# Performance work log

Hardware: AMD Instinct MI355X
Metric: run time of the kernel (lower is better)

The kernel has to match this reference:

```python
import jax, jax.numpy as jnp
import numpy as np

STATE_DIM = 28224  # 84*84*4 flattened Atari stack
N_EPISODE = 8192
FEATURE_DIM = 32
K_NEAREST = 10
C = 0.001
EPS_KERNEL = 0.001


def setup_inputs() -> dict:
    key = jax.random.key(0)
    ks = jax.random.split(key, 5)
    s = jax.random.normal(ks[0], (1, STATE_DIM), dtype=jnp.float32)
    episode = jax.random.normal(ks[1], (N_EPISODE, STATE_DIM), dtype=jnp.float32)
    dm2 = jnp.ones((1,), dtype=jnp.float32)  # running distance stat (torch inits 0.0; 1.0 avoids div-by-zero)
    # fan-in scaled weights so activations stay O(1)
    W1 = jax.random.normal(ks[2], (STATE_DIM, 128), dtype=jnp.float32) / np.sqrt(STATE_DIM)
    b1 = jnp.zeros((128,), dtype=jnp.float32)
    W2 = jax.random.normal(ks[3], (128, 64), dtype=jnp.float32) / np.sqrt(128.0)
    b2 = jnp.zeros((64,), dtype=jnp.float32)
    W3 = jax.random.normal(ks[4], (64, FEATURE_DIM), dtype=jnp.float32) / np.sqrt(64.0)
    b3 = jnp.zeros((FEATURE_DIM,), dtype=jnp.float32)
    return {"s": s, "episode": episode, "dm2": dm2,
            "W1": W1, "b1": b1, "W2": W2, "b2": b2, "W3": W3, "b3": b3}


def _embed(x, W1, b1, W2, b2, W3, b3):
    h = jax.nn.relu(x @ W1 + b1)
    h = jax.nn.relu(h @ W2 + b2)
    return h @ W3 + b3  # [*, FEATURE_DIM]


def reference(s, episode, dm2, W1, b1, W2, b2, W3, b3):
    z_s = _embed(s, W1, b1, W2, b2, W3, b3)          # [1, F]
    z_ep = _embed(episode, W1, b1, W2, b2, W3, b3)   # [N, F]
    dist = jnp.linalg.norm(z_s - z_ep, axis=1)       # [N]
    kernel = EPS_KERNEL / (dist / dm2[0] + EPS_KERNEL)
    top_k_kernel, _ = jax.lax.top_k(kernel, K_NEAREST)           # largest kernel values
    neg_top_dist, _ = jax.lax.top_k(-dist, K_NEAREST)            # smallest distances
    top_k_dist = -neg_top_dist
    new_dm2 = 0.99 * dm2[0] + 0.01 * jnp.mean(top_k_dist)        # running-stat update
    reward_episodic = 1.0 / (jnp.sqrt(jnp.mean(top_k_kernel)) + C)
    return reward_episodic, new_dm2
```

## Files before the change

kernel.cpp:

```cpp
#include <hip/hip_runtime.h>
#include <hip/hip_bf16.h>

typedef __attribute__((ext_vector_type(8))) __bf16 bf16x8;
typedef __attribute__((ext_vector_type(4))) float f32x4;
typedef __attribute__((ext_vector_type(4))) unsigned short u16x4;

#define STATE_DIM 28224
#define NEP 8192
#define MPAD 8320
#define KSPLIT 7
#define KSTEPS 63
#define BK 64
#define EPSK 0.001f
#define CC 0.001f

#define WT_BYTES   (441 * 8192 * 2)
#define PART_BYTES (KSPLIT * MPAD * 128 * 4)
#define Z_BYTES    (MPAD * 32 * 4)
#define DIST_BYTES (NEP * 4)
#define WS_NEEDED  (WT_BYTES + PART_BYTES + Z_BYTES + DIST_BYTES)

__device__ __forceinline__ unsigned short f2bf(float f) {
    unsigned int u = __float_as_uint(f);
    u += 0x7fffu + ((u >> 16) & 1u);
    return (unsigned short)(u >> 16);
}

__device__ __forceinline__ void glds16(const void* g, void* l) {
    __builtin_amdgcn_global_load_lds(
        (const __attribute__((address_space(1))) unsigned int*)g,
        (__attribute__((address_space(3))) unsigned int*)l, 16, 0, 0);
}

__global__ __launch_bounds__(256) void prep_wt(const float* __restrict__ W1,
                                               unsigned short* __restrict__ WtS) {
    __shared__ __align__(16) unsigned short img[8192];
    const int c = blockIdx.x;
    const int tid = threadIdx.x;
    const int k0 = c * 64;
#pragma unroll
    for (int i = 0; i < 32; ++i) {
        const int f = i * 256 + tid;
        const int k = f >> 7, n = f & 127;
        const float wv = W1[(size_t)(k0 + k) * 128 + n];
        const int ad = ((n * 128 + k * 2) ^ ((n & 7) << 4)) >> 1;
        img[ad] = f2bf(wv);
    }
    __syncthreads();
    unsigned short* dst = WtS + (size_t)c * 8192;
#pragma unroll
    for (int i = 0; i < 4; ++i) {
        const int f = i * 256 + tid;
        *reinterpret_cast<uint4*>(dst + f * 8) =
            *reinterpret_cast<const uint4*>(img + f * 8);
    }
}

__global__ __launch_bounds__(256, 3) void gemm1(const float* __restrict__ ep,
                                                const float* __restrict__ s,
                                                const unsigned short* __restrict__ WtS,
                                                float* __restrict__ part) {
    __shared__ __align__(16) unsigned char smA[128 * 64 * 2];
    __shared__ __align__(16) unsigned char smB[2][128 * 64 * 2];

    const int bid = blockIdx.x;
    const int ks = bid / 65;
    const int mt = bid % 65;
    const int tid = threadIdx.x;
    const int kBase = ks * (KSTEPS * BK);
    const int chunkBase = ks * KSTEPS;

    const int mBase = tid >> 4;
    const int kOff = (tid & 15) * 4;
    const int swzW = (mBase & 7) << 4;

    const bool last = (mt == 64);
    const int rowBase = mt * 128;

    float4 aR[8];

    auto loadA = [&](int kc) {
#pragma unroll
        for (int i = 0; i < 8; ++i) {
            const int m = mBase + i * 16;
            const int rg = rowBase + m;
            if (!last) {
                aR[i] = *reinterpret_cast<const float4*>(ep + (size_t)rg * STATE_DIM + kc + kOff);
            } else {
                if (rg < NEP)
                    aR[i] = *reinterpret_cast<const float4*>(ep + (size_t)rg * STATE_DIM + kc + kOff);
                else if (rg == NEP)
                    aR[i] = *reinterpret_cast<const float4*>(s + kc + kOff);
                else
                    aR[i] = make_float4(0.f, 0.f, 0.f, 0.f);
            }
        }
    };

    const int w = tid >> 6;
    const int lane = tid & 63;

    auto stageB = [&](int chunkIdx, int buf) {
        const char* cb = (const char*)(WtS + (size_t)chunkIdx * 8192);
#pragma unroll
        for (int r2 = 0; r2 < 4; ++r2) {
            const int off = ((r2 << 2) + w) << 10;
            glds16(cb + off + (lane << 4), &smB[buf][off]);
        }
    };

    auto writeLdsA = [&]() {
#pragma unroll
        for (int i = 0; i < 8; ++i) {
            const int m = mBase + i * 16;
            u16x4 av;
            av[0] = f2bf(aR[i].x); av[1] = f2bf(aR[i].y);
            av[2] = f2bf(aR[i].z); av[3] = f2bf(aR[i].w);
            const int ad = (m * 128 + kOff * 2) ^ swzW;
            *reinterpret_cast<u16x4*>(smA + ad) = av;
        }
    };

    const int wr = w >> 1, wc = w & 1;
    const int l15 = lane & 15, lq = lane >> 4;
    const int swzF = (l15 & 7) << 4;

    f32x4 acc[4][4] = {};

    auto compute = [&](int buf) {
#pragma unroll
        for (int kh = 0; kh < 2; ++kh) {
            bf16x8 af[4], bf[4];
#pragma unroll
            for (int mf = 0; mf < 4; ++mf) {
                const int row = wr * 64 + mf * 16 + l15;
                const int ad = (row * 128 + (kh * 32 + lq * 8) * 2) ^ swzF;
                af[mf] = *reinterpret_cast<const bf16x8*>(smA + ad);
            }
#pragma unroll
            for (int nf = 0; nf < 4; ++nf) {
                const int row = wc * 64 + nf * 16 + l15;
                const int ad = (row * 128 + (kh * 32 + lq * 8) * 2) ^ swzF;
                bf[nf] = *reinterpret_cast<const bf16x8*>(smB[buf] + ad);
            }
#pragma unroll
            for (int mf = 0; mf < 4; ++mf)
#pragma unroll
                for (int nf = 0; nf < 4; ++nf)
                    acc[mf][nf] = __builtin_amdgcn_mfma_f32_16x16x32_bf16(
                        af[mf], bf[nf], acc[mf][nf], 0, 0, 0);
        }
    };

    loadA(kBase);
    stageB(chunkBase, 0);
    int buf = 0;
    for (int t2 = 0; t2 < KSTEPS; ++t2) {
        __syncthreads();
        writeLdsA();
        __syncthreads();
        if (t2 + 1 < KSTEPS) {
            loadA(kBase + (t2 + 1) * BK);
            stageB(chunkBase + t2 + 1, buf ^ 1);
        }
        compute(buf);
        buf ^= 1;
    }

    float* po = part + ((size_t)ks * MPAD + rowBase) * 128;
#pragma unroll
    for (int mf = 0; mf < 4; ++mf)
#pragma unroll
        for (int nf = 0; nf < 4; ++nf)
#pragma unroll
            for (int v = 0; v < 4; ++v) {
                const int row = wr * 64 + mf * 16 + lq * 4 + v;
                const int col = wc * 64 + nf * 16 + l15;
                po[(size_t)row * 128 + col] = acc[mf][nf][v];
            }
}

__global__ __launch_bounds__(256) void mlp23(const float* __restrict__ part,
                                             const float* __restrict__ b1,
                                             const float* __restrict__ W2,
                                             const float* __restrict__ b2,
                                             const float* __restrict__ W3,
                                             const float* __restrict__ b3,
                                             float* __restrict__ z) {
    __shared__ float W2t[64 * 129];
    __shared__ float W3t[32 * 65];
    __shared__ float b1L[128], b2L[64], b3L[32];
    __shared__ float h1buf[4][128];
    __shared__ float h2buf[4][64];

    const int tid = threadIdx.x;
#pragma unroll
    for (int i = 0; i < 32; ++i) {
        int f = tid + i * 256;
        W2t[(f & 63) * 129 + (f >> 6)] = W2[f];
    }
#pragma unroll
    for (int i = 0; i < 8; ++i) {
        int f = tid + i * 256;
        W3t[(f & 31) * 65 + (f >> 5)] = W3[f];
    }
    if (tid < 128) b1L[tid] = b1[tid];
    if (tid < 64) b2L[tid] = b2[tid];
    if (tid < 32) b3L[tid] = b3[tid];
    __syncthreads();

    const int w = tid >> 6, l = tid & 63;
    const int base = blockIdx.x * 16 + w * 4;
    for (int rr = 0; rr < 4; ++rr) {
        const int r = base + rr;
        if (r > NEP) continue;
        float h1a = b1L[l], h1b = b1L[l + 64];
#pragma unroll
        for (int p = 0; p < KSPLIT; ++p) {
            const float* pp = part + ((size_t)p * MPAD + r) * 128;
            h1a += pp[l];
            h1b += pp[l + 64];
        }
        h1a = fmaxf(h1a, 0.f);
        h1b = fmaxf(h1b, 0.f);
        h1buf[w][l] = h1a;
        h1buf[w][l + 64] = h1b;
        float s0 = 0.f, s1 = 0.f, s2 = 0.f, s3 = 0.f;
        const float* wr2 = &W2t[l * 129];
        const float* hb = h1buf[w];
#pragma unroll 8
        for (int k = 0; k < 32; ++k) {
            s0 += hb[k]      * wr2[k];
            s1 += hb[k + 32] * wr2[k + 32];
            s2 += hb[k + 64] * wr2[k + 64];
            s3 += hb[k + 96] * wr2[k + 96];
        }
        float a2 = fmaxf(b2L[l] + ((s0 + s1) + (s2 + s3)), 0.f);
        h2buf[w][l] = a2;
        const int c = l & 31;
        const float* wr3 = &W3t[c * 65];
        const float* h2 = h2buf[w];
        float t0 = 0.f, t1 = 0.f;
#pragma unroll 8
        for (int k = 0; k < 32; ++k) {
            t0 += h2[k]      * wr3[k];
            t1 += h2[k + 32] * wr3[k + 32];
        }
        if (l < 32) z[(size_t)r * 32 + c] = b3L[c] + t0 + t1;
    }
}

__global__ __launch_bounds__(256) void dist_k(const float* __restrict__ z,
                                              float* __restrict__ dist) {
    __shared__ float zs[32];
    const int t = threadIdx.x;
    if (t < 32) zs[t] = z[(size_t)NEP * 32 + t];
    __syncthreads();
    const int r = blockIdx.x * 256 + t;
    const float* zr = z + (size_t)r * 32;
    float d2 = 0.f;
#pragma unroll
    for (int c2 = 0; c2 < 32; ++c2) {
        const float d = zr[c2] - zs[c2];
        d2 += d * d;
    }
    dist[r] = sqrtf(d2);
}

__global__ __launch_bounds__(256) void top10_k(const float* __restrict__ dist,
                                               const float* __restrict__ dm2,
                                               float* __restrict__ out) {
    const int t = threadIdx.x;
    float v[32];
#pragma unroll
    for (int i = 0; i < 32; ++i) v[i] = dist[i * 256 + t];

    __shared__ float wv[4];
    __shared__ int wi[4];

    const float dm = dm2[0];
    float sd = 0.f, sk = 0.f;

    for (int round = 0; round < 10; ++round) {
        float bv = 3.0e38f;
        int bi = 0x7fffffff;
#pragma unroll
        for (int i = 0; i < 32; ++i) {
            const float x = v[i];
            const int idx = i * 256 + t;
            if (x < bv) { bv = x; bi = idx; }
        }
#pragma unroll
        for (int sft = 1; sft < 64; sft <<= 1) {
            const float ov = __shfl_xor(bv, sft);
            const int oi = __shfl_xor(bi, sft);
            if (ov < bv || (ov == bv && oi < bi)) { bv = ov; bi = oi; }
        }
        const int wid = t >> 6;
        if ((t & 63) == 0) { wv[wid] = bv; wi[wid] = bi; }
        __syncthreads();
        bv = wv[0]; bi = wi[0];
#pragma unroll
        for (int k = 1; k < 4; ++k) {
            const float ov = wv[k]; const int oi = wi[k];
            if (ov < bv || (ov == bv && oi < bi)) { bv = ov; bi = oi; }
        }
        __syncthreads();
#pragma unroll
        for (int i = 0; i < 32; ++i)
            if (bi == i * 256 + t) v[i] = 3.0e38f;
        sd += bv;
        sk += EPSK / (bv / dm + EPSK);
    }

    if (t == 0) {
        const float meand = sd * 0.1f;
        const float meank = sk * 0.1f;
        out[0] = 1.0f / (sqrtf(meank) + CC);
        out[1] = 0.99f * dm + 0.01f * meand;
    }
}

extern "C" void kernel_launch(void* const* d_in, const int* in_sizes, int n_in,
                              void* d_out, int out_size, void* d_ws, size_t ws_size,
                              hipStream_t stream) {
    const float* s   = (const float*)d_in[0];
    const float* ep  = (const float*)d_in[1];
    const float* dm2 = (const float*)d_in[2];
    const float* W1  = (const float*)d_in[3];
    const float* b1  = (const float*)d_in[4];
    const float* W2  = (const float*)d_in[5];
    const float* b2  = (const float*)d_in[6];
    const float* W3  = (const float*)d_in[7];
    const float* b3  = (const float*)d_in[8];
    float* out = (float*)d_out;

    if (ws_size < (size_t)WS_NEEDED) return;

    unsigned short* WtS = (unsigned short*)d_ws;
    float* part = (float*)((char*)d_ws + WT_BYTES);
    float* zbuf = (float*)((char*)d_ws + WT_BYTES + PART_BYTES);
    float* dist = (float*)((char*)d_ws + WT_BYTES + PART_BYTES + Z_BYTES);

    hipLaunchKernelGGL(prep_wt, dim3(441), dim3(256), 0, stream, W1, WtS);
    hipLaunchKernelGGL(gemm1, dim3(65 * KSPLIT), dim3(256), 0, stream, ep, s, WtS, part);
    hipLaunchKernelGGL(mlp23, dim3(MPAD / 16), dim3(256), 0, stream, part, b1, W2, b2, W3, b3, zbuf);
    hipLaunchKernelGGL(dist_k, dim3(32), dim3(256), 0, stream, zbuf, dist);
    hipLaunchKernelGGL(top10_k, dim3(1), dim3(256), 0, stream, dist, dm2, out);
}
```

Baseline: 241.4 us.

## Store GEMM1 split-K partials as bf16 and remap workgroups across XCDs

```diff
diff --git a/kernel.cpp b/kernel.cpp
--- a/kernel.cpp
+++ b/kernel.cpp
@@ -11,11 +11,12 @@
 #define KSPLIT 7
 #define KSTEPS 63
 #define BK 64
+#define NWG (65 * KSPLIT)
 #define EPSK 0.001f
 #define CC 0.001f
 
 #define WT_BYTES   (441 * 8192 * 2)
-#define PART_BYTES (KSPLIT * MPAD * 128 * 4)
+#define PART_BYTES (KSPLIT * MPAD * 128 * 2)
 #define Z_BYTES    (MPAD * 32 * 4)
 #define DIST_BYTES (NEP * 4)
 #define WS_NEEDED  (WT_BYTES + PART_BYTES + Z_BYTES + DIST_BYTES)
@@ -56,14 +57,18 @@
     }
 }
 
-__global__ __launch_bounds__(256, 3) void gemm1(const float* __restrict__ ep,
+__global__ __launch_bounds__(256, 2) void gemm1(const float* __restrict__ ep,
                                                 const float* __restrict__ s,
                                                 const unsigned short* __restrict__ WtS,
-                                                float* __restrict__ part) {
+                                                unsigned short* __restrict__ part) {
     __shared__ __align__(16) unsigned char smA[128 * 64 * 2];
     __shared__ __align__(16) unsigned char smB[2][128 * 64 * 2];
 
-    const int bid = blockIdx.x;
+    const int hw = blockIdx.x;
+    const int xcd = hw & 7, slot = hw >> 3;
+    const int q = NWG >> 3, r = NWG & 7;
+    const int bid = (xcd < r ? xcd * (q + 1) : r * (q + 1) + (xcd - r) * q) + slot;
+
     const int ks = bid / 65;
     const int mt = bid % 65;
     const int tid = threadIdx.x;
@@ -167,7 +172,7 @@
         buf ^= 1;
     }
 
-    float* po = part + ((size_t)ks * MPAD + rowBase) * 128;
+    unsigned short* po = part + ((size_t)ks * MPAD + rowBase) * 128;
 #pragma unroll
     for (int mf = 0; mf < 4; ++mf)
 #pragma unroll
@@ -176,11 +181,11 @@
             for (int v = 0; v < 4; ++v) {
                 const int row = wr * 64 + mf * 16 + lq * 4 + v;
                 const int col = wc * 64 + nf * 16 + l15;
-                po[(size_t)row * 128 + col] = acc[mf][nf][v];
+                po[(size_t)row * 128 + col] = f2bf(acc[mf][nf][v]);
             }
 }
 
-__global__ __launch_bounds__(256) void mlp23(const float* __restrict__ part,
+__global__ __launch_bounds__(256) void mlp23(const unsigned short* __restrict__ part,
                                              const float* __restrict__ b1,
                                              const float* __restrict__ W2,
                                              const float* __restrict__ b2,
@@ -209,22 +214,22 @@
     if (tid < 32) b3L[tid] = b3[tid];
     __syncthreads();
 
+    const unsigned int* pu = (const unsigned int*)part;
     const int w = tid >> 6, l = tid & 63;
     const int base = blockIdx.x * 16 + w * 4;
     for (int rr = 0; rr < 4; ++rr) {
         const int r = base + rr;
         if (r > NEP) continue;
-        float h1a = b1L[l], h1b = b1L[l + 64];
+        float h1a = b1L[2 * l], h1b = b1L[2 * l + 1];
 #pragma unroll
         for (int p = 0; p < KSPLIT; ++p) {
-            const float* pp = part + ((size_t)p * MPAD + r) * 128;
-            h1a += pp[l];
-            h1b += pp[l + 64];
+            const unsigned int u = pu[((size_t)p * MPAD + r) * 64 + l];
+            h1a += __uint_as_float(u << 16);
+            h1b += __uint_as_float(u & 0xffff0000u);
         }
         h1a = fmaxf(h1a, 0.f);
         h1b = fmaxf(h1b, 0.f);
-        h1buf[w][l] = h1a;
-        h1buf[w][l + 64] = h1b;
+        *reinterpret_cast<float2*>(&h1buf[w][2 * l]) = make_float2(h1a, h1b);
         float s0 = 0.f, s1 = 0.f, s2 = 0.f, s3 = 0.f;
         const float* wr2 = &W2t[l * 129];
         const float* hb = h1buf[w];
@@ -337,13 +342,13 @@
 
     if (ws_size < (size_t)WS_NEEDED) return;
 
-    unsigned short* WtS = (unsigned short*)d_ws;
-    float* part = (float*)((char*)d_ws + WT_BYTES);
+    unsigned short* WtS  = (unsigned short*)d_ws;
+    unsigned short* part = (unsigned short*)((char*)d_ws + WT_BYTES);
     float* zbuf = (float*)((char*)d_ws + WT_BYTES + PART_BYTES);
     float* dist = (float*)((char*)d_ws + WT_BYTES + PART_BYTES + Z_BYTES);
 
     hipLaunchKernelGGL(prep_wt, dim3(441), dim3(256), 0, stream, W1, WtS);
-    hipLaunchKernelGGL(gemm1, dim3(65 * KSPLIT), dim3(256), 0, stream, ep, s, WtS, part);
+    hipLaunchKernelGGL(gemm1, dim3(NWG), dim3(256), 0, stream, ep, s, WtS, part);
     hipLaunchKernelGGL(mlp23, dim3(MPAD / 16), dim3(256), 0, stream, part, b1, W2, b2, W3, b3, zbuf);
     hipLaunchKernelGGL(dist_k, dim3(32), dim3(256), 0, stream, zbuf, dist);
     hipLaunchKernelGGL(top10_k, dim3(1), dim3(256), 0, stream, dist, dm2, out);
```

Result: faster. 227.8 us (-5.6%).
